# Performance work log

Measured on AMD Instinct MI355X. Metric: run time of the kernel, lower is better.

Reference implementation:

```python
import jax, jax.numpy as jnp
import numpy as np

B, L, W = 4096, 30, 5          # batch, MAX_TOKEN_LENGTH, WINDOW_SIZE
A, E = 30, 128                 # ALPHABET_SIZE, embedding dim
C = 40                         # OUT_CHANNELS
H, T = 128, 3                  # LSTM_UNITS, num CRF tags
LIN = W * C                    # 200
EPS = 1e-5


def setup_inputs():
    key = jax.random.key(0)
    ks = jax.random.split(key, 24)
    def rn(k, shape, s=0.1):
        return jax.random.normal(k, shape, jnp.float32) * s
    return {
        'x': jax.random.randint(ks[0], (B, L, W), 0, A, jnp.int32),
        'emb': rn(ks[1], (A, E), 1.0),
        'conv_w': rn(ks[2], (C, E, 3)),
        'conv_b': rn(ks[3], (C,)),
        'bn1_g': 1.0 + rn(ks[4], (C,)),
        'bn1_b': rn(ks[5], (C,)),
        'bn1_m': rn(ks[6], (C,)),
        'bn1_v': 0.5 + jax.random.uniform(ks[7], (C,), jnp.float32),
        'w_ih_f': rn(ks[8], (4 * H, LIN)),
        'w_hh_f': rn(ks[9], (4 * H, H)),
        'b_f': rn(ks[10], (4 * H,)),
        'w_ih_b': rn(ks[11], (4 * H, LIN)),
        'w_hh_b': rn(ks[12], (4 * H, H)),
        'b_b': rn(ks[13], (4 * H,)),
        'bn2_g': 1.0 + rn(ks[14], (2 * H,)),
        'bn2_b': rn(ks[15], (2 * H,)),
        'bn2_m': rn(ks[16], (2 * H,)),
        'bn2_v': 0.5 + jax.random.uniform(ks[17], (2 * H,), jnp.float32),
        'fc_w': rn(ks[18], (T, 2 * H)),
        'fc_b': rn(ks[19], (T,)),
        'trans': rn(ks[20], (T, T)),
        'start_t': rn(ks[21], (T,)),
        'end_t': rn(ks[22], (T,)),
    }


def _lstm_dir(seq, w_ih, w_hh, b, reverse):
    # seq: [B, L, F]; torch gate order i, f, g, o
    xs = jnp.einsum('blf,gf->lbg', seq, w_ih) + b  # [L, B, 4H]
    h0 = jnp.zeros((seq.shape[0], H), seq.dtype)
    def step(carry, xt):
        h, c = carry
        z = xt + h @ w_hh.T
        i, f, g, o = jnp.split(z, 4, axis=-1)
        c = jax.nn.sigmoid(f) * c + jax.nn.sigmoid(i) * jnp.tanh(g)
        h = jax.nn.sigmoid(o) * jnp.tanh(c)
        return (h, c), h
    _, hs = jax.lax.scan(step, (h0, h0), xs, reverse=reverse)
    return hs.transpose(1, 0, 2)  # [B, L, H]


def _viterbi(emis, mask, trans, start_t, end_t):
    # emis: [B, L, T], mask: [B, L] bool
    score = start_t + emis[:, 0]                      # [B, T]
    def step(score, inp):
        e_t, m_t = inp                                # [B, T], [B]
        cand = score[:, :, None] + trans              # [B, Tprev, Tnext]
        ptr = jnp.argmax(cand, axis=1)                # [B, T]
        new = jnp.max(cand, axis=1) + e_t
        return jnp.where(m_t[:, None], new, score), ptr
    score, hist = jax.lax.scan(
        step, score, (emis[:, 1:].transpose(1, 0, 2), mask[:, 1:].T))
    score = score + end_t
    best = jnp.max(score, axis=1)                     # [B] path scores
    last = jnp.argmax(score, axis=1)                  # [B]
    def back(tag, inp):
        h_t, m_t = inp
        prev = jnp.take_along_axis(h_t, tag[:, None], axis=1)[:, 0]
        tag = jnp.where(m_t, prev, tag)
        return tag, tag
    _, ys = jax.lax.scan(back, last, (hist, mask[:, 1:].T), reverse=True)
    tags = jnp.concatenate([ys, last[None]], axis=0).T  # [B, L]
    return best, tags


def reference(x, emb, conv_w, conv_b, bn1_g, bn1_b, bn1_m, bn1_v,
              w_ih_f, w_hh_f, b_f, w_ih_b, w_hh_b, b_b,
              bn2_g, bn2_b, bn2_m, bn2_v, fc_w, fc_b, trans, start_t, end_t):
    mask = x[:, :, 2] > 0                             # [B, L]
    e = emb[x.reshape(B * L, W)]                      # [N, W, E]  (dropout=eval noop)
    e = e.transpose(0, 2, 1)                          # [N, E, W]
    y = jax.lax.conv_general_dilated(
        e, conv_w, (1,), [(1, 1)],
        dimension_numbers=('NCH', 'OIH', 'NCH')) + conv_b[:, None]
    # BatchNorm1d (inference, running stats)
    y = (y - bn1_m[:, None]) * (bn1_g / jnp.sqrt(bn1_v + EPS))[:, None] + bn1_b[:, None]
    y = jax.nn.relu(y)
    # MaxPool1d(k=3, stride=1, pad=1): length preserved
    y = jax.lax.reduce_window(y, -jnp.inf, jax.lax.max,
                              (1, 1, 3), (1, 1, 1),
                              [(0, 0), (0, 0), (1, 1)])
    y = y.reshape(B, L, LIN)                          # torch.flatten is channel-major = row-major reshape
    hf = _lstm_dir(y, w_ih_f, w_hh_f, b_f, False)
    hb = _lstm_dir(y, w_ih_b, w_hh_b, b_b, True)
    h = jnp.concatenate([hf, hb], axis=-1)            # [B, L, 2H]
    h = (h - bn2_m) * (bn2_g / jnp.sqrt(bn2_v + EPS)) + bn2_b
    emis = h @ fc_w.T + fc_b                          # [B, L, T]
    return _viterbi(emis, mask, trans, start_t, end_t)
```

## Files before the change

### kernel.cpp

```cpp
#include <hip/hip_runtime.h>
#include <math.h>

#define BB    4096
#define LL    30
#define WW    5
#define CC    40
#define HH    128
#define TT    3
#define KA    328
#define NB    32
#define FSTR  232
#define HSTR  136
#define CW    1056

#define WS_P    0
#define WS_BC   3600
#define WS_BG   3648
#define WS_WFC  4672
#define WS_EB   5440
#define WS_WBF  5504
#define WS_EMIS (5504 + 540672)

typedef __bf16 bf16x8 __attribute__((ext_vector_type(8)));
typedef float  f32x4  __attribute__((ext_vector_type(4)));
typedef unsigned short u16x8 __attribute__((ext_vector_type(8)));

__device__ __forceinline__ float sigm(float x) {
    return __builtin_amdgcn_rcpf(1.0f + __expf(-x));
}
__device__ __forceinline__ float tanh_fast(float x) {
    return 2.0f * __builtin_amdgcn_rcpf(1.0f + __expf(-2.0f * x)) - 1.0f;
}
__device__ __forceinline__ unsigned short f2bf(float f) {
    unsigned u = __builtin_bit_cast(unsigned, f);
    return (unsigned short)((u + 0x7FFFu + ((u >> 16) & 1u)) >> 16);
}
__device__ __forceinline__ float bf2f(unsigned short h) {
    unsigned u = ((unsigned)h) << 16;
    return __builtin_bit_cast(float, u);
}

__global__ void prep_kernel(const float* __restrict__ emb, const float* __restrict__ conv_w,
                            const float* __restrict__ conv_b,
                            const float* __restrict__ bn1_g, const float* __restrict__ bn1_b,
                            const float* __restrict__ bn1_m, const float* __restrict__ bn1_v,
                            const float* __restrict__ w_ih_f, const float* __restrict__ w_hh_f,
                            const float* __restrict__ b_f,
                            const float* __restrict__ w_ih_b, const float* __restrict__ w_hh_b,
                            const float* __restrict__ b_b,
                            const float* __restrict__ bn2_g, const float* __restrict__ bn2_b,
                            const float* __restrict__ bn2_m, const float* __restrict__ bn2_v,
                            const float* __restrict__ fc_w, const float* __restrict__ fc_b,
                            float* __restrict__ ws)
{
    const int gid = blockIdx.x * blockDim.x + threadIdx.x;
    const int gsz = gridDim.x * blockDim.x;

    for (int idx = gid; idx < 3600; idx += gsz) {
        int k = idx / 1200, rem = idx % 1200, a = rem / 40, c = rem % 40;
        float s1 = bn1_g[c] / sqrtf(bn1_v[c] + 1e-5f);
        float acc = 0.f;
        for (int e = 0; e < 128; ++e)
            acc += emb[a * 128 + e] * conv_w[(c * 128 + e) * 3 + k];
        ws[WS_P + idx] = acc * s1;
    }
    for (int c = gid; c < CC; c += gsz) {
        float s1 = bn1_g[c] / sqrtf(bn1_v[c] + 1e-5f);
        ws[WS_BC + c] = (conv_b[c] - bn1_m[c]) * s1 + bn1_b[c];
    }
    for (int i = gid; i < 1024; i += gsz) {
        int d = i >> 9, g = i & 511;
        ws[WS_BG + i] = d ? b_b[g] : b_f[g];
    }
    for (int i = gid; i < 768; i += gsz) {
        int d = i / 384, r = i % 384, t = r / 128, u = r % 128;
        int j = d * 128 + u;
        float s2 = bn2_g[j] / sqrtf(bn2_v[j] + 1e-5f);
        ws[WS_WFC + i] = fc_w[t * 256 + j] * s2;
    }
    for (int t = gid; t < TT; t += gsz) {
        float acc = fc_b[t];
        for (int j = 0; j < 256; ++j) {
            float s2 = bn2_g[j] / sqrtf(bn2_v[j] + 1e-5f);
            acc += fc_w[t * 256 + j] * (bn2_b[j] - bn2_m[j] * s2);
        }
        ws[WS_EB + t] = acc;
    }
    unsigned short* wsu = (unsigned short*)ws;
    for (int i = gid; i < 2 * 512 * CW; i += gsz) {
        int d = i / (512 * CW), r = i % (512 * CW);
        int n = r / CW, q = r % CW;
        int Ks = q / 96, t = q % 96, s = t / 32, k32 = t % 32;
        int k = Ks * 32 + k32;
        int u = n >> 2, g = n & 3, row = g * 128 + u;
        const float* wih = d ? w_ih_b : w_ih_f;
        const float* whh = d ? w_hh_b : w_hh_f;
        float w = (k < 200) ? wih[row * 200 + k]
                            : ((k >= 224) ? whh[row * 128 + (k - 224)] : 0.f);
        unsigned short t0 = f2bf(w);
        float r1 = w - bf2f(t0);
        unsigned short t1 = f2bf(r1);
        unsigned short t2 = f2bf(r1 - bf2f(t1));
        wsu[2 * WS_WBF + i] = (s == 0) ? t0 : ((s == 1) ? t1 : t2);
    }
}

__global__ __launch_bounds__(512, 1)
void lstm_kernel(const int* __restrict__ x, float* __restrict__ ws)
{
    __shared__ unsigned short Fh[2][NB * FSTR], Fl[2][NB * FSTR], Fm[2][NB * FSTR];
    __shared__ unsigned short Hh[NB * HSTR], Hl[NB * HSTR], Hm[NB * HSTR];
    __shared__ float Pp_s[3600];
    __shared__ float Wfc_s[384];
    __shared__ float biasC_s[40];

    const int tid = threadIdx.x;
    const int d   = blockIdx.x & 1;
    const int b0  = (blockIdx.x >> 1) * NB;

    const unsigned short* __restrict__ Wb =
        (const unsigned short*)ws + 2 * WS_WBF + d * (512 * CW);
    float* emis = ws + WS_EMIS + d * (BB * LL * TT);

    for (int i = tid; i < 3600; i += 512) Pp_s[i] = ws[WS_P + i];
    for (int i = tid; i < 384;  i += 512) Wfc_s[i] = ws[WS_WFC + d * 384 + i];
    for (int i = tid; i < 40;   i += 512) biasC_s[i] = ws[WS_BC + i];
    for (int i = tid; i < NB * FSTR; i += 512) {
        ((unsigned*)Fh)[i] = 0u; ((unsigned*)Fl)[i] = 0u; ((unsigned*)Fm)[i] = 0u;
    }
    for (int i = tid; i < NB * HSTR / 2; i += 512) {
        ((unsigned*)Hh)[i] = 0u; ((unsigned*)Hl)[i] = 0u; ((unsigned*)Hm)[i] = 0u;
    }

    const int lane = tid & 63;
    const int wv   = tid >> 6;
    const int quad = lane >> 4;
    const int ml   = lane & 15;

    const unsigned short* __restrict__ Wn0 = Wb + (wv * 64 +  0 + ml) * CW + quad * 8;
    const unsigned short* __restrict__ Wn1 = Wb + (wv * 64 + 16 + ml) * CW + quad * 8;
    const unsigned short* __restrict__ Wn2 = Wb + (wv * 64 + 32 + ml) * CW + quad * 8;
    const unsigned short* __restrict__ Wn3 = Wb + (wv * 64 + 48 + ml) * CW + quad * 8;

    const float* bgp = ws + WS_BG + d * 512;
    int   un[4];
    float bIv[4], bFv[4], bGv[4], bOv[4];
    #pragma unroll
    for (int nt = 0; nt < 4; ++nt) {
        int u = wv * 16 + nt * 4 + quad;
        un[nt]  = u;
        bIv[nt] = bgp[u];
        bFv[nt] = bgp[128 + u];
        bGv[nt] = bgp[256 + u];
        bOv[nt] = bgp[384 + u];
    }

    float cst[2][4];
    #pragma unroll
    for (int mt = 0; mt < 2; ++mt)
        #pragma unroll
        for (int nt = 0; nt < 4; ++nt) cst[mt][nt] = 0.f;

    __syncthreads();

#define DO_FEATURES(LPOS, BUF)                                                 \
    for (int p = tid; p < NB * CC; p += 512) {                                 \
        int bb = p / CC, c = p % CC;                                           \
        const int* tok = x + (((b0 + bb) * LL) + (LPOS)) * WW;                 \
        int t0 = tok[0], t1 = tok[1], t2 = tok[2], t3 = tok[3], t4 = tok[4];   \
        float bc = biasC_s[c];                                                 \
        float a0 = bc + Pp_s[(30 + t0) * 40 + c] + Pp_s[(60 + t1) * 40 + c];   \
        float a1 = bc + Pp_s[t0 * 40 + c] + Pp_s[(30 + t1) * 40 + c] + Pp_s[(60 + t2) * 40 + c]; \
        float a2 = bc + Pp_s[t1 * 40 + c] + Pp_s[(30 + t2) * 40 + c] + Pp_s[(60 + t3) * 40 + c]; \
        float a3 = bc + Pp_s[t2 * 40 + c] + Pp_s[(30 + t3) * 40 + c] + Pp_s[(60 + t4) * 40 + c]; \
        float a4 = bc + Pp_s[t3 * 40 + c] + Pp_s[(30 + t4) * 40 + c];          \
        a0 = fmaxf(a0, 0.f); a1 = fmaxf(a1, 0.f); a2 = fmaxf(a2, 0.f);         \
        a3 = fmaxf(a3, 0.f); a4 = fmaxf(a4, 0.f);                              \
        float f[5];                                                            \
        f[0] = fmaxf(a0, a1);                                                  \
        f[1] = fmaxf(fmaxf(a0, a1), a2);                                       \
        f[2] = fmaxf(fmaxf(a1, a2), a3);                                       \
        f[3] = fmaxf(fmaxf(a2, a3), a4);                                       \
        f[4] = fmaxf(a3, a4);                                                  \
        int base = bb * FSTR + c * 5;                                          \
        _Pragma("unroll")                                                      \
        for (int j = 0; j < 5; ++j) {                                          \
            unsigned short h0 = f2bf(f[j]);                                    \
            float r1 = f[j] - bf2f(h0);                                        \
            unsigned short h1 = f2bf(r1);                                      \
            unsigned short h2 = f2bf(r1 - bf2f(h1));                           \
            Fh[BUF][base + j] = h0;                                            \
            Fl[BUF][base + j] = h1;                                            \
            Fm[BUF][base + j] = h2;                                            \
        }                                                                      \
    }

    {
        const int l0 = d ? (LL - 1) : 0;
        DO_FEATURES(l0, 0)
    }
    __syncthreads();

    for (int step = 0; step < LL; ++step) {
        const int fb = step & 1;

        f32x4 acc[2][4];
        #pragma unroll
        for (int mt = 0; mt < 2; ++mt)
            #pragma unroll
            for (int nt = 0; nt < 4; ++nt)
                acc[mt][nt] = (f32x4){0.f, 0.f, 0.f, 0.f};

#define WLOAD(B, P, KS)                                                        \
        {                                                                      \
            B[0] = *(const bf16x8*)((P) + (KS) * 96);                          \
            B[1] = *(const bf16x8*)((P) + (KS) * 96 + 32);                     \
            B[2] = *(const bf16x8*)((P) + (KS) * 96 + 64);                     \
        }
#define GEMM6(B, NT)                                                           \
        {                                                                      \
            acc[0][NT] = __builtin_amdgcn_mfma_f32_16x16x32_bf16(B[0], a0[0], acc[0][NT], 0, 0, 0); \
            acc[0][NT] = __builtin_amdgcn_mfma_f32_16x16x32_bf16(B[0], a0[1], acc[0][NT], 0, 0, 0); \
            acc[0][NT] = __builtin_amdgcn_mfma_f32_16x16x32_bf16(B[1], a0[0], acc[0][NT], 0, 0, 0); \
            acc[0][NT] = __builtin_amdgcn_mfma_f32_16x16x32_bf16(B[1], a0[1], acc[0][NT], 0, 0, 0); \
            acc[0][NT] = __builtin_amdgcn_mfma_f32_16x16x32_bf16(B[2], a0[0], acc[0][NT], 0, 0, 0); \
            acc[0][NT] = __builtin_amdgcn_mfma_f32_16x16x32_bf16(B[0], a0[2], acc[0][NT], 0, 0, 0); \
            acc[1][NT] = __builtin_amdgcn_mfma_f32_16x16x32_bf16(B[0], a1[0], acc[1][NT], 0, 0, 0); \
            acc[1][NT] = __builtin_amdgcn_mfma_f32_16x16x32_bf16(B[0], a1[1], acc[1][NT], 0, 0, 0); \
            acc[1][NT] = __builtin_amdgcn_mfma_f32_16x16x32_bf16(B[1], a1[0], acc[1][NT], 0, 0, 0); \
            acc[1][NT] = __builtin_amdgcn_mfma_f32_16x16x32_bf16(B[1], a1[1], acc[1][NT], 0, 0, 0); \
            acc[1][NT] = __builtin_amdgcn_mfma_f32_16x16x32_bf16(B[2], a1[0], acc[1][NT], 0, 0, 0); \
            acc[1][NT] = __builtin_amdgcn_mfma_f32_16x16x32_bf16(B[0], a1[2], acc[1][NT], 0, 0, 0); \
        }

        {
            bf16x8 bufA[3], bufB[3];
            WLOAD(bufA, Wn0, 0)

            #pragma unroll
            for (int Ks = 0; Ks < 11; ++Ks) {
                bf16x8 a0[3], a1[3];
                if (Ks < 7) {
                    const int ko = Ks * 32 + quad * 8;
                    a0[0] = *(const bf16x8*)&Fh[fb][ml * FSTR + ko];
                    a0[1] = *(const bf16x8*)&Fl[fb][ml * FSTR + ko];
                    a0[2] = *(const bf16x8*)&Fm[fb][ml * FSTR + ko];
                    a1[0] = *(const bf16x8*)&Fh[fb][(16 + ml) * FSTR + ko];
                    a1[1] = *(const bf16x8*)&Fl[fb][(16 + ml) * FSTR + ko];
                    a1[2] = *(const bf16x8*)&Fm[fb][(16 + ml) * FSTR + ko];
                } else {
                    const int ko = (Ks - 7) * 32 + quad * 8;
                    a0[0] = *(const bf16x8*)&Hh[ml * HSTR + ko];
                    a0[1] = *(const bf16x8*)&Hl[ml * HSTR + ko];
                    a0[2] = *(const bf16x8*)&Hm[ml * HSTR + ko];
                    a1[0] = *(const bf16x8*)&Hh[(16 + ml) * HSTR + ko];
                    a1[1] = *(const bf16x8*)&Hl[(16 + ml) * HSTR + ko];
                    a1[2] = *(const bf16x8*)&Hm[(16 + ml) * HSTR + ko];
                }
                WLOAD(bufB, Wn1, Ks)
                GEMM6(bufA, 0)
                WLOAD(bufA, Wn2, Ks)
                GEMM6(bufB, 1)
                WLOAD(bufB, Wn3, Ks)
                GEMM6(bufA, 2)
                if (Ks < 10) WLOAD(bufA, Wn0, Ks + 1)
                GEMM6(bufB, 3)
            }
        }
#undef WLOAD
#undef GEMM6

        if (step + 1 < LL) {
            const int lnext = d ? (LL - 2 - step) : (step + 1);
            DO_FEATURES(lnext, (step + 1) & 1)
        }
        if (step > 0 && tid < 192) {
            const int lprev = d ? (LL - step) : (step - 1);
            int bb = tid / 6, r6 = tid % 6, t = r6 >> 1, seg = r6 & 1;
            int hb = bb * HSTR + seg * 64;
            const float* wfc = &Wfc_s[t * 128 + seg * 64];
            float s = 0.f;
            #pragma unroll
            for (int i = 0; i < 8; ++i) {
                u16x8 v0 = *(const u16x8*)&Hh[hb + i * 8];
                u16x8 v1 = *(const u16x8*)&Hl[hb + i * 8];
                u16x8 v2 = *(const u16x8*)&Hm[hb + i * 8];
                #pragma unroll
                for (int j = 0; j < 8; ++j) {
                    float h = bf2f(v0[j]) + bf2f(v1[j]) + bf2f(v2[j]);
                    s += h * wfc[i * 8 + j];
                }
            }
            s += __shfl_xor(s, 1);
            if (seg == 0)
                emis[(((b0 + bb) * LL) + lprev) * TT + t] = s;
        }

        __syncthreads();

        #pragma unroll
        for (int mt = 0; mt < 2; ++mt) {
            #pragma unroll
            for (int nt = 0; nt < 4; ++nt) {
                float zi = acc[mt][nt][0] + bIv[nt];
                float zf = acc[mt][nt][1] + bFv[nt];
                float zg = acc[mt][nt][2] + bGv[nt];
                float zo = acc[mt][nt][3] + bOv[nt];
                float cn = sigm(zf) * cst[mt][nt] + sigm(zi) * tanh_fast(zg);
                cst[mt][nt] = cn;
                float h = sigm(zo) * tanh_fast(cn);
                unsigned short h0 = f2bf(h);
                float r1 = h - bf2f(h0);
                unsigned short h1 = f2bf(r1);
                unsigned short h2 = f2bf(r1 - bf2f(h1));
                int idx = (mt * 16 + ml) * HSTR + un[nt];
                Hh[idx] = h0;
                Hl[idx] = h1;
                Hm[idx] = h2;
            }
        }
        __syncthreads();
    }

    if (tid < 192) {
        const int llast = d ? 0 : (LL - 1);
        int bb = tid / 6, r6 = tid % 6, t = r6 >> 1, seg = r6 & 1;
        int hb = bb * HSTR + seg * 64;
        const float* wfc = &Wfc_s[t * 128 + seg * 64];
        float s = 0.f;
        #pragma unroll
        for (int i = 0; i < 8; ++i) {
            u16x8 v0 = *(const u16x8*)&Hh[hb + i * 8];
            u16x8 v1 = *(const u16x8*)&Hl[hb + i * 8];
            u16x8 v2 = *(const u16x8*)&Hm[hb + i * 8];
            #pragma unroll
            for (int j = 0; j < 8; ++j) {
                float h = bf2f(v0[j]) + bf2f(v1[j]) + bf2f(v2[j]);
                s += h * wfc[i * 8 + j];
            }
        }
        s += __shfl_xor(s, 1);
        if (seg == 0)
            emis[(((b0 + bb) * LL) + llast) * TT + t] = s;
    }
#undef DO_FEATURES
}

__global__ void viterbi_kernel(const int* __restrict__ x, const float* __restrict__ ws,
                               const float* __restrict__ trans,
                               const float* __restrict__ start_t,
                               const float* __restrict__ end_t,
                               float* __restrict__ out)
{
    int b = blockIdx.x * blockDim.x + threadIdx.x;
    if (b >= BB) return;
    const float* eF = ws + WS_EMIS;
    const float* eB = ws + WS_EMIS + BB * LL * TT;
    const float eb0 = ws[WS_EB + 0], eb1 = ws[WS_EB + 1], eb2 = ws[WS_EB + 2];
    float tr[9];
    #pragma unroll
    for (int i = 0; i < 9; ++i) tr[i] = trans[i];

    int base = b * LL * TT;
    float s0 = start_t[0] + eF[base + 0] + eB[base + 0] + eb0;
    float s1 = start_t[1] + eF[base + 1] + eB[base + 1] + eb1;
    float s2 = start_t[2] + eF[base + 2] + eB[base + 2] + eb2;

    unsigned hist[LL - 1];
    unsigned maskbits = 0;

    #pragma unroll
    for (int l = 1; l < LL; ++l) {
        bool m = x[(b * LL + l) * WW + 2] > 0;
        if (m) maskbits |= (1u << l);
        int idx = base + l * TT;
        float e0 = eF[idx + 0] + eB[idx + 0] + eb0;
        float e1 = eF[idx + 1] + eB[idx + 1] + eb1;
        float e2 = eF[idx + 2] + eB[idx + 2] + eb2;

        float ns[3]; int pt[3];
        #pragma unroll
        for (int nt = 0; nt < 3; ++nt) {
            float c0 = s0 + tr[0 * 3 + nt];
            float c1 = s1 + tr[1 * 3 + nt];
            float c2 = s2 + tr[2 * 3 + nt];
            int p = 0; float bc = c0;
            if (c1 > bc) { bc = c1; p = 1; }
            if (c2 > bc) { bc = c2; p = 2; }
            ns[nt] = bc; pt[nt] = p;
        }
        ns[0] += e0; ns[1] += e1; ns[2] += e2;
        hist[l - 1] = (unsigned)pt[0] | ((unsigned)pt[1] << 2) | ((unsigned)pt[2] << 4);
        if (m) { s0 = ns[0]; s1 = ns[1]; s2 = ns[2]; }
    }
    s0 += end_t[0]; s1 += end_t[1]; s2 += end_t[2];
    float best = s0; int last = 0;
    if (s1 > best) { best = s1; last = 1; }
    if (s2 > best) { best = s2; last = 2; }

    out[b] = best;
    float* tags = out + BB + b * LL;
    int tag = last;
    tags[LL - 1] = (float)last;
    #pragma unroll
    for (int l = LL - 1; l >= 1; --l) {
        int prev = (int)((hist[l - 1] >> (2 * tag)) & 3u);
        if (maskbits & (1u << l)) tag = prev;
        tags[l - 1] = (float)tag;
    }
}

extern "C" void kernel_launch(void* const* d_in, const int* in_sizes, int n_in,
                              void* d_out, int out_size, void* d_ws, size_t ws_size,
                              hipStream_t stream)
{
    const int*   x      = (const int*)  d_in[0];
    const float* emb    = (const float*)d_in[1];
    const float* conv_w = (const float*)d_in[2];
    const float* conv_b = (const float*)d_in[3];
    const float* bn1_g  = (const float*)d_in[4];
    const float* bn1_b  = (const float*)d_in[5];
    const float* bn1_m  = (const float*)d_in[6];
    const float* bn1_v  = (const float*)d_in[7];
    const float* w_ih_f = (const float*)d_in[8];
    const float* w_hh_f = (const float*)d_in[9];
    const float* b_f    = (const float*)d_in[10];
    const float* w_ih_b = (const float*)d_in[11];
    const float* w_hh_b = (const float*)d_in[12];
    const float* b_b    = (const float*)d_in[13];
    const float* bn2_g  = (const float*)d_in[14];
    const float* bn2_b  = (const float*)d_in[15];
    const float* bn2_m  = (const float*)d_in[16];
    const float* bn2_v  = (const float*)d_in[17];
    const float* fc_w   = (const float*)d_in[18];
    const float* fc_b   = (const float*)d_in[19];
    const float* trans  = (const float*)d_in[20];
    const float* start_t= (const float*)d_in[21];
    const float* end_t  = (const float*)d_in[22];

    float* ws  = (float*)d_ws;
    float* out = (float*)d_out;

    prep_kernel<<<256, 256, 0, stream>>>(emb, conv_w, conv_b,
                                         bn1_g, bn1_b, bn1_m, bn1_v,
                                         w_ih_f, w_hh_f, b_f,
                                         w_ih_b, w_hh_b, b_b,
                                         bn2_g, bn2_b, bn2_m, bn2_v,
                                         fc_w, fc_b, ws);
    lstm_kernel<<<256, 512, 0, stream>>>(x, ws);
    viterbi_kernel<<<16, 256, 0, stream>>>(x, ws, trans, start_t, end_t, out);
}
```

Before: 808.6 us.

## Halve LSTM batch tile to 16 and launch twice as many blocks

Shrinks the per-block batch tile from 32 to 16 rows, which removes the second M-tile of MFMA accumulators and doubles the grid from 256 to 512 blocks. It also raises the launch-bounds minimum to 4 blocks per CU. The aim is to fill more of the GPU's compute units and shorten each recurrent step's serial critical path. In exchange, every block reloads the full recurrent weight matrix from global/L2, so each weight load feeds half as many MFMAs and total weight traffic doubles.

```diff
diff --git a/kernel.cpp b/kernel.cpp
--- a/kernel.cpp
+++ b/kernel.cpp
@@ -8,7 +8,7 @@
 #define HH    128
 #define TT    3
 #define KA    328
-#define NB    32
+#define NB    16
 #define FSTR  232
 #define HSTR  136
 #define CW    1056
@@ -105,7 +105,7 @@
     }
 }
 
-__global__ __launch_bounds__(512, 1)
+__global__ __launch_bounds__(512, 4)
 void lstm_kernel(const int* __restrict__ x, float* __restrict__ ws)
 {
     __shared__ unsigned short Fh[2][NB * FSTR], Fl[2][NB * FSTR], Fm[2][NB * FSTR];
@@ -155,11 +155,9 @@
         bOv[nt] = bgp[384 + u];
     }
 
-    float cst[2][4];
+    float cst[4];
     #pragma unroll
-    for (int mt = 0; mt < 2; ++mt)
-        #pragma unroll
-        for (int nt = 0; nt < 4; ++nt) cst[mt][nt] = 0.f;
+    for (int nt = 0; nt < 4; ++nt) cst[nt] = 0.f;
 
     __syncthreads();
 
@@ -204,12 +202,10 @@
     for (int step = 0; step < LL; ++step) {
         const int fb = step & 1;
 
-        f32x4 acc[2][4];
+        f32x4 acc[4];
         #pragma unroll
-        for (int mt = 0; mt < 2; ++mt)
-            #pragma unroll
-            for (int nt = 0; nt < 4; ++nt)
-                acc[mt][nt] = (f32x4){0.f, 0.f, 0.f, 0.f};
+        for (int nt = 0; nt < 4; ++nt)
+            acc[nt] = (f32x4){0.f, 0.f, 0.f, 0.f};
 
 #define WLOAD(B, P, KS)                                                        \
         {                                                                      \
@@ -219,18 +215,12 @@
         }
 #define GEMM6(B, NT)                                                           \
         {                                                                      \
-            acc[0][NT] = __builtin_amdgcn_mfma_f32_16x16x32_bf16(B[0], a0[0], acc[0][NT], 0, 0, 0); \
-            acc[0][NT] = __builtin_amdgcn_mfma_f32_16x16x32_bf16(B[0], a0[1], acc[0][NT], 0, 0, 0); \
-            acc[0][NT] = __builtin_amdgcn_mfma_f32_16x16x32_bf16(B[1], a0[0], acc[0][NT], 0, 0, 0); \
-            acc[0][NT] = __builtin_amdgcn_mfma_f32_16x16x32_bf16(B[1], a0[1], acc[0][NT], 0, 0, 0); \
-            acc[0][NT] = __builtin_amdgcn_mfma_f32_16x16x32_bf16(B[2], a0[0], acc[0][NT], 0, 0, 0); \
-            acc[0][NT] = __builtin_amdgcn_mfma_f32_16x16x32_bf16(B[0], a0[2], acc[0][NT], 0, 0, 0); \
-            acc[1][NT] = __builtin_amdgcn_mfma_f32_16x16x32_bf16(B[0], a1[0], acc[1][NT], 0, 0, 0); \
-            acc[1][NT] = __builtin_amdgcn_mfma_f32_16x16x32_bf16(B[0], a1[1], acc[1][NT], 0, 0, 0); \
-            acc[1][NT] = __builtin_amdgcn_mfma_f32_16x16x32_bf16(B[1], a1[0], acc[1][NT], 0, 0, 0); \
-            acc[1][NT] = __builtin_amdgcn_mfma_f32_16x16x32_bf16(B[1], a1[1], acc[1][NT], 0, 0, 0); \
-            acc[1][NT] = __builtin_amdgcn_mfma_f32_16x16x32_bf16(B[2], a1[0], acc[1][NT], 0, 0, 0); \
-            acc[1][NT] = __builtin_amdgcn_mfma_f32_16x16x32_bf16(B[0], a1[2], acc[1][NT], 0, 0, 0); \
+            acc[NT] = __builtin_amdgcn_mfma_f32_16x16x32_bf16(B[0], a0[0], acc[NT], 0, 0, 0); \
+            acc[NT] = __builtin_amdgcn_mfma_f32_16x16x32_bf16(B[0], a0[1], acc[NT], 0, 0, 0); \
+            acc[NT] = __builtin_amdgcn_mfma_f32_16x16x32_bf16(B[1], a0[0], acc[NT], 0, 0, 0); \
+            acc[NT] = __builtin_amdgcn_mfma_f32_16x16x32_bf16(B[1], a0[1], acc[NT], 0, 0, 0); \
+            acc[NT] = __builtin_amdgcn_mfma_f32_16x16x32_bf16(B[2], a0[0], acc[NT], 0, 0, 0); \
+            acc[NT] = __builtin_amdgcn_mfma_f32_16x16x32_bf16(B[0], a0[2], acc[NT], 0, 0, 0); \
         }
 
         {
@@ -239,23 +229,17 @@
 
             #pragma unroll
             for (int Ks = 0; Ks < 11; ++Ks) {
-                bf16x8 a0[3], a1[3];
+                bf16x8 a0[3];
                 if (Ks < 7) {
                     const int ko = Ks * 32 + quad * 8;
                     a0[0] = *(const bf16x8*)&Fh[fb][ml * FSTR + ko];
                     a0[1] = *(const bf16x8*)&Fl[fb][ml * FSTR + ko];
                     a0[2] = *(const bf16x8*)&Fm[fb][ml * FSTR + ko];
-                    a1[0] = *(const bf16x8*)&Fh[fb][(16 + ml) * FSTR + ko];
-                    a1[1] = *(const bf16x8*)&Fl[fb][(16 + ml) * FSTR + ko];
-                    a1[2] = *(const bf16x8*)&Fm[fb][(16 + ml) * FSTR + ko];
                 } else {
                     const int ko = (Ks - 7) * 32 + quad * 8;
                     a0[0] = *(const bf16x8*)&Hh[ml * HSTR + ko];
                     a0[1] = *(const bf16x8*)&Hl[ml * HSTR + ko];
                     a0[2] = *(const bf16x8*)&Hm[ml * HSTR + ko];
-                    a1[0] = *(const bf16x8*)&Hh[(16 + ml) * HSTR + ko];
-                    a1[1] = *(const bf16x8*)&Hl[(16 + ml) * HSTR + ko];
-                    a1[2] = *(const bf16x8*)&Hm[(16 + ml) * HSTR + ko];
                 }
                 WLOAD(bufB, Wn1, Ks)
                 GEMM6(bufA, 0)
@@ -274,7 +258,7 @@
             const int lnext = d ? (LL - 2 - step) : (step + 1);
             DO_FEATURES(lnext, (step + 1) & 1)
         }
-        if (step > 0 && tid < 192) {
+        if (step > 0 && tid < NB * 6) {
             const int lprev = d ? (LL - step) : (step - 1);
             int bb = tid / 6, r6 = tid % 6, t = r6 >> 1, seg = r6 & 1;
             int hb = bb * HSTR + seg * 64;
@@ -299,30 +283,27 @@
         __syncthreads();
 
         #pragma unroll
-        for (int mt = 0; mt < 2; ++mt) {
-            #pragma unroll
-            for (int nt = 0; nt < 4; ++nt) {
-                float zi = acc[mt][nt][0] + bIv[nt];
-                float zf = acc[mt][nt][1] + bFv[nt];
-                float zg = acc[mt][nt][2] + bGv[nt];
-                float zo = acc[mt][nt][3] + bOv[nt];
-                float cn = sigm(zf) * cst[mt][nt] + sigm(zi) * tanh_fast(zg);
-                cst[mt][nt] = cn;
-                float h = sigm(zo) * tanh_fast(cn);
-                unsigned short h0 = f2bf(h);
-                float r1 = h - bf2f(h0);
-                unsigned short h1 = f2bf(r1);
-                unsigned short h2 = f2bf(r1 - bf2f(h1));
-                int idx = (mt * 16 + ml) * HSTR + un[nt];
-                Hh[idx] = h0;
-                Hl[idx] = h1;
-                Hm[idx] = h2;
-            }
+        for (int nt = 0; nt < 4; ++nt) {
+            float zi = acc[nt][0] + bIv[nt];
+            float zf = acc[nt][1] + bFv[nt];
+            float zg = acc[nt][2] + bGv[nt];
+            float zo = acc[nt][3] + bOv[nt];
+            float cn = sigm(zf) * cst[nt] + sigm(zi) * tanh_fast(zg);
+            cst[nt] = cn;
+            float h = sigm(zo) * tanh_fast(cn);
+            unsigned short h0 = f2bf(h);
+            float r1 = h - bf2f(h0);
+            unsigned short h1 = f2bf(r1);
+            unsigned short h2 = f2bf(r1 - bf2f(h1));
+            int idx = ml * HSTR + un[nt];
+            Hh[idx] = h0;
+            Hl[idx] = h1;
+            Hm[idx] = h2;
         }
         __syncthreads();
     }
 
-    if (tid < 192) {
+    if (tid < NB * 6) {
         const int llast = d ? 0 : (LL - 1);
         int bb = tid / 6, r6 = tid % 6, t = r6 >> 1, seg = r6 & 1;
         int hb = bb * HSTR + seg * 64;
@@ -447,6 +428,6 @@
                                          w_ih_b, w_hh_b, b_b,
                                          bn2_g, bn2_b, bn2_m, bn2_v,
                                          fc_w, fc_b, ws);
-    lstm_kernel<<<256, 512, 0, stream>>>(x, ws);
+    lstm_kernel<<<512, 512, 0, stream>>>(x, ws);
     viterbi_kernel<<<16, 256, 0, stream>>>(x, ws, trans, start_t, end_t, out);
 }
```

Measured after the change: 1.204 ms. 1.49x slower.
